# Kernel tuning notes

Measured on AMD Instinct MI355X. Metric: run time of the kernel, lower is better.

The kernel has to match this reference:

```python
import jax, jax.numpy as jnp
import numpy as np

B, C, H, W = 16, 512, 64, 64
SCALE = 8
CQK = C // SCALE  # 64
EPS = 1e-6


def setup_inputs() -> dict:
    key = jax.random.key(0)
    ks = jax.random.split(key, 8)
    x = jax.random.normal(ks[0], (B, C, H, W), dtype=jnp.float32)
    # 1x1 conv weights stored as [out_ch, in_ch] (kernel_size=1)
    Wq = jax.random.normal(ks[1], (CQK, C), dtype=jnp.float32) * 0.02
    bq = jnp.zeros((CQK,), dtype=jnp.float32)
    Wk = jax.random.normal(ks[2], (CQK, C), dtype=jnp.float32) * 0.02
    bk = jnp.zeros((CQK,), dtype=jnp.float32)
    Wv = jax.random.normal(ks[3], (C, C), dtype=jnp.float32) * 0.02
    bv = jnp.zeros((C,), dtype=jnp.float32)
    # gamma is initialized to 0 in the module; use a nonzero value so the
    # output is non-trivial for kernel correctness checks.
    gamma = jax.random.normal(ks[4], (1,), dtype=jnp.float32)
    return {"x": x, "Wq": Wq, "bq": bq, "Wk": Wk, "bk": bk,
            "Wv": Wv, "bv": bv, "gamma": gamma}


def _l2norm_ch(t):
    # normalize over the channel axis (dim=-2), matching torch.norm(p=2, dim=-2)
    nrm = jnp.sqrt(jnp.sum(t * t, axis=-2, keepdims=True))
    return t / jnp.maximum(nrm, EPS)


def reference(x, Wq, bq, Wk, bk, Wv, bv, gamma):
    b, c, h, w = x.shape
    n = h * w
    xf = x.reshape(b, c, n)                                   # [B,C,N]
    # 1x1 convs == channel matmuls
    Q = jnp.einsum('oc,bcn->bon', Wq, xf) + bq[None, :, None]  # [B,cqk,N]
    K = jnp.einsum('oc,bcn->bon', Wk, xf) + bk[None, :, None]  # [B,cqk,N]
    V = jnp.einsum('oc,bcn->bon', Wv, xf) + bv[None, :, None]  # [B,C,N]
    Qn = _l2norm_ch(Q).transpose(0, 2, 1)                      # [B,N,cqk]
    Kn = _l2norm_ch(K)                                         # [B,cqk,N]
    # Taylor-softmax surrogate denominator
    denom = n + jnp.einsum('bnc,bc->bn', Qn, Kn.sum(axis=-1))  # [B,N]
    tailor = 1.0 / jnp.maximum(denom, 1e-6)                    # [B,N]
    # KtV accumulation: [B,cqk,C]
    matrix = jnp.einsum('bmn,bcn->bmc', Kn, V)
    value_sum = jnp.sum(V, axis=-1)[:, :, None]                # [B,C,1] -> broadcast
    matrix_sum = value_sum + jnp.einsum('bnm,bmc->bcn', Qn, matrix)  # [B,C,N]
    weight_value = matrix_sum * tailor[:, None, :]             # [B,C,N]
    out = gamma * weight_value.reshape(b, c, h, w)
    return jnp.nan_to_num(out, nan=0.0, posinf=1.0, neginf=-1.0)
```

## Files before the change

kernel.cpp:

```cpp
#include <hip/hip_runtime.h>


typedef __attribute__((ext_vector_type(8))) short short8_t;
typedef __attribute__((ext_vector_type(4))) float f32x4;

__device__ __forceinline__ unsigned short f2bf(float f) {
  union { float f; unsigned u; } v; v.f = f;
  unsigned r = v.u + 0x7FFFu + ((v.u >> 16) & 1u);
  return (unsigned short)(r >> 16);
}
__device__ __forceinline__ float bf2f(unsigned short h) {
  union { unsigned u; float f; } v; v.u = ((unsigned)h) << 16;
  return v.f;
}

#define MFMA(a, b, c) __builtin_amdgcn_mfma_f32_16x16x32_bf16((a), (b), (c), 0, 0, 0)

__global__ void k_prep(const float* __restrict__ Wq, const float* __restrict__ Wk,
                       unsigned short* __restrict__ Wqk) {
  int idx = blockIdx.x * 256 + threadIdx.x;
  int o = idx >> 9, c = idx & 511;
  float v = (o < 64) ? Wq[o * 512 + c] : Wk[(o - 64) * 512 + c];
  Wqk[idx] = f2bf(v);
}

__launch_bounds__(256, 2)
__global__ void k_qk(const float* __restrict__ x, const unsigned short* __restrict__ Wqk,
                     const float* __restrict__ bq, const float* __restrict__ bk,
                     unsigned short* __restrict__ QnT, unsigned short* __restrict__ KnG,
                     float* __restrict__ Ksum) {
  __shared__ __align__(16) unsigned char smem[39424];
  unsigned short* SA = (unsigned short*)smem;
  unsigned short* SB = (unsigned short*)(smem + 10240);
  unsigned short* EQ = (unsigned short*)smem;
  unsigned short* EK = (unsigned short*)(smem + 18432);
  float* ssq   = (float*)(smem + 35840);
  float* invq  = (float*)(smem + 37888);
  float* invk  = (float*)(smem + 38400);
  float* biasL = (float*)(smem + 38912);

  const int t = threadIdx.x;
  const int lane = t & 63, w = t >> 6;
  const int l15 = lane & 15, quad = lane >> 4;
  const int nt = blockIdx.x, b = blockIdx.y;
  const int n0 = nt * 128;
  const float* xb = x + (size_t)b * 512 * 4096;

  if (t < 128) biasL[t] = (t < 64) ? bq[t] : bk[t - 64];

  f32x4 acc[2][8];
#pragma unroll
  for (int i = 0; i < 2; ++i)
#pragma unroll
    for (int j = 0; j < 8; ++j) acc[i][j] = (f32x4){0.f, 0.f, 0.f, 0.f};

  const int nB = t & 127;
  const int cgB = t >> 7;

  for (int kc = 0; kc < 16; ++kc) {
    const int c0 = kc * 32;
    __syncthreads();
#pragma unroll
    for (int p = 0; p < 2; ++p) {
      int idx = t + p * 256;
      int o = idx >> 2, seg = idx & 3;
      *(short8_t*)(SA + o * 40 + seg * 8) =
          *(const short8_t*)(Wqk + o * 512 + c0 + seg * 8);
    }
#pragma unroll
    for (int g = 0; g < 2; ++g) {
      int cb = c0 + cgB * 8 + g * 16;
      const float* src = xb + (size_t)cb * 4096 + n0 + nB;
      short8_t v;
#pragma unroll
      for (int i = 0; i < 8; ++i) v[i] = (short)f2bf(src[(size_t)i * 4096]);
      *(short8_t*)(SB + nB * 40 + cgB * 8 + g * 16) = v;
    }
    __syncthreads();
    short8_t a0 = *(const short8_t*)(SA + (w * 32 + l15) * 40 + quad * 8);
    short8_t a1 = *(const short8_t*)(SA + (w * 32 + 16 + l15) * 40 + quad * 8);
#pragma unroll
    for (int tc = 0; tc < 8; ++tc) {
      short8_t bfr = *(const short8_t*)(SB + (tc * 16 + l15) * 40 + quad * 8);
      acc[0][tc] = MFMA(a0, bfr, acc[0][tc]);
      acc[1][tc] = MFMA(a1, bfr, acc[1][tc]);
    }
  }
  __syncthreads();

#pragma unroll
  for (int trl = 0; trl < 2; ++trl)
#pragma unroll
    for (int reg = 0; reg < 4; ++reg) {
      int o = w * 32 + trl * 16 + quad * 4 + reg;
      float bias = biasL[o];
#pragma unroll
      for (int tc = 0; tc < 8; ++tc) acc[trl][tc][reg] += bias;
    }

#pragma unroll
  for (int tc = 0; tc < 8; ++tc) {
    float v = 0.f;
#pragma unroll
    for (int trl = 0; trl < 2; ++trl)
#pragma unroll
      for (int reg = 0; reg < 4; ++reg) {
        float q = acc[trl][tc][reg];
        v += q * q;
      }
    v += __shfl_xor(v, 16);
    v += __shfl_xor(v, 32);
    if (quad == 0) ssq[w * 128 + tc * 16 + l15] = v;
  }
  __syncthreads();
  if (t < 128) {
    float qs = ssq[t] + ssq[128 + t];
    float ks = ssq[256 + t] + ssq[384 + t];
    invq[t] = 1.0f / fmaxf(sqrtf(qs), 1e-6f);
    invk[t] = 1.0f / fmaxf(sqrtf(ks), 1e-6f);
  }
  __syncthreads();

  if (w < 2) {
#pragma unroll
    for (int trl = 0; trl < 2; ++trl)
#pragma unroll
      for (int tc = 0; tc < 8; ++tc) {
        int n = tc * 16 + l15;
        float inv = invq[n];
#pragma unroll
        for (int reg = 0; reg < 4; ++reg) {
          int o = w * 32 + trl * 16 + quad * 4 + reg;
          EQ[n * 72 + o] = f2bf(acc[trl][tc][reg] * inv);
        }
      }
  } else {
#pragma unroll
    for (int trl = 0; trl < 2; ++trl)
#pragma unroll
      for (int reg = 0; reg < 4; ++reg) {
        int m = (w - 2) * 32 + trl * 16 + quad * 4 + reg;
        float p = 0.f;
#pragma unroll
        for (int tc = 0; tc < 8; ++tc) {
          int n = tc * 16 + l15;
          float val = acc[trl][tc][reg] * invk[n];
          EK[m * 136 + n] = f2bf(val);
          p += val;
        }
        p += __shfl_xor(p, 1);
        p += __shfl_xor(p, 2);
        p += __shfl_xor(p, 4);
        p += __shfl_xor(p, 8);
        if (l15 == 0) atomicAdd(Ksum + b * 64 + m, p);
      }
  }
  __syncthreads();

  unsigned short* qdst = QnT + ((size_t)b * 4096 + n0) * 64;
#pragma unroll
  for (int p = 0; p < 4; ++p) {
    int idx = t + p * 256;
    int row = idx >> 3, seg = idx & 7;
    *(short8_t*)(qdst + row * 64 + seg * 8) = *(const short8_t*)(EQ + row * 72 + seg * 8);
  }
  unsigned short* kdst = KnG + (size_t)b * 64 * 4096 + n0;
#pragma unroll
  for (int p = 0; p < 4; ++p) {
    int idx = t + p * 256;
    int row = idx >> 4, seg = idx & 15;
    *(short8_t*)(kdst + (size_t)row * 4096 + seg * 8) =
        *(const short8_t*)(EK + row * 136 + seg * 8);
  }
}

__launch_bounds__(256, 2)
__global__ void k_t(const float* __restrict__ x, const unsigned short* __restrict__ KnG,
                    float* __restrict__ T, float* __restrict__ xsum) {
  __shared__ __align__(16) unsigned char smem[15360];
  unsigned short* SA = (unsigned short*)smem;
  unsigned short* SB = (unsigned short*)(smem + 5120);
  const int t = threadIdx.x;
  const int lane = t & 63, w = t >> 6;
  const int l15 = lane & 15, quad = lane >> 4;
  const int ns = blockIdx.x, ct = blockIdx.y, b = blockIdx.z;
  const int c0 = ct * 128;
  const float* xb = x + (size_t)b * 512 * 4096;
  const unsigned short* Knb = KnG + (size_t)b * 64 * 4096;

  f32x4 acc[4][2];
#pragma unroll
  for (int i = 0; i < 4; ++i)
#pragma unroll
    for (int j = 0; j < 2; ++j) acc[i][j] = (f32x4){0.f, 0.f, 0.f, 0.f};

  const int crow = t >> 1, half = t & 1;
  float xs = 0.f;

  for (int ch = 0; ch < 16; ++ch) {
    const int nb = ns * 512 + ch * 32;
    __syncthreads();
    {
      int m = t >> 2, seg = t & 3;
      *(short8_t*)(SA + m * 40 + seg * 8) =
          *(const short8_t*)(Knb + (size_t)m * 4096 + nb + seg * 8);
    }
    {
      const float* src = xb + (size_t)(c0 + crow) * 4096 + nb + half * 16;
      const f32x4* s4 = (const f32x4*)src;
      f32x4 f0 = s4[0], f1 = s4[1], f2 = s4[2], f3 = s4[3];
      short8_t v0, v1;
#pragma unroll
      for (int i = 0; i < 4; ++i) { xs += f0[i]; v0[i] = (short)f2bf(f0[i]); }
#pragma unroll
      for (int i = 0; i < 4; ++i) { xs += f1[i]; v0[4 + i] = (short)f2bf(f1[i]); }
#pragma unroll
      for (int i = 0; i < 4; ++i) { xs += f2[i]; v1[i] = (short)f2bf(f2[i]); }
#pragma unroll
      for (int i = 0; i < 4; ++i) { xs += f3[i]; v1[4 + i] = (short)f2bf(f3[i]); }
      *(short8_t*)(SB + crow * 40 + half * 16)     = v0;
      *(short8_t*)(SB + crow * 40 + half * 16 + 8) = v1;
    }
    __syncthreads();
    short8_t af[4];
#pragma unroll
    for (int tm = 0; tm < 4; ++tm)
      af[tm] = *(const short8_t*)(SA + (tm * 16 + l15) * 40 + quad * 8);
#pragma unroll
    for (int tcl = 0; tcl < 2; ++tcl) {
      short8_t bfr = *(const short8_t*)(SB + (w * 32 + tcl * 16 + l15) * 40 + quad * 8);
#pragma unroll
      for (int tm = 0; tm < 4; ++tm) acc[tm][tcl] = MFMA(af[tm], bfr, acc[tm][tcl]);
    }
  }
  xs += __shfl_xor(xs, 1);
  if (half == 0) atomicAdd(xsum + b * 512 + c0 + crow, xs);
#pragma unroll
  for (int tm = 0; tm < 4; ++tm)
#pragma unroll
    for (int tcl = 0; tcl < 2; ++tcl)
#pragma unroll
      for (int reg = 0; reg < 4; ++reg) {
        int m = tm * 16 + quad * 4 + reg;
        int c = c0 + w * 32 + tcl * 16 + l15;
        atomicAdd(T + ((size_t)b * 64 + m) * 512 + c, acc[tm][tcl][reg]);
      }
}

__launch_bounds__(256, 2)
__global__ void k_mat(const float* __restrict__ T, const float* __restrict__ Wv,
                      const float* __restrict__ bv, const float* __restrict__ xsum,
                      const float* __restrict__ Ksum,
                      unsigned short* __restrict__ matT, float* __restrict__ Vsum) {
  __shared__ __align__(16) unsigned char smem[27136];
  float* ST = (float*)smem;
  float* SW = (float*)(smem + 17408);
  float* SV = (float*)(smem + 26112);
  const int t = threadIdx.x;
  const int cb = blockIdx.x, b = blockIdx.y;
  const int c0 = cb * 32;
  const int m = t >> 2, cs = t & 3;
  float acc[8] = {0.f, 0.f, 0.f, 0.f, 0.f, 0.f, 0.f, 0.f};

  for (int kc = 0; kc < 8; ++kc) {
    __syncthreads();
#pragma unroll
    for (int p = 0; p < 4; ++p) {
      int idx = t + p * 256;
      int row = idx >> 4, f4 = idx & 15;
      *(f32x4*)(ST + row * 68 + f4 * 4) =
          *(const f32x4*)(T + ((size_t)b * 64 + row) * 512 + kc * 64 + f4 * 4);
    }
#pragma unroll
    for (int p = 0; p < 2; ++p) {
      int idx = t + p * 256;
      int row = idx >> 4, f4 = idx & 15;
      *(f32x4*)(SW + row * 68 + f4 * 4) =
          *(const f32x4*)(Wv + (size_t)(c0 + row) * 512 + kc * 64 + f4 * 4);
    }
    __syncthreads();
    for (int kk = 0; kk < 64; ++kk) {
      float tv = ST[m * 68 + kk];
#pragma unroll
      for (int j = 0; j < 8; ++j) acc[j] += tv * SW[(cs + j * 4) * 68 + kk];
    }
  }
  float ks = Ksum[b * 64 + m];
#pragma unroll
  for (int j = 0; j < 8; ++j) {
    int c = c0 + cs + j * 4;
    float mv = acc[j] + bv[c] * ks;
    matT[((size_t)b * 512 + c) * 64 + m] = f2bf(mv);
  }
  {
    int cc = t >> 3, kp = t & 7;
    const float* wr = Wv + (size_t)(c0 + cc) * 512 + kp * 64;
    const float* xr = xsum + b * 512 + kp * 64;
    float s = 0.f;
    for (int i = 0; i < 64; ++i) s += wr[i] * xr[i];
    SV[cc * 8 + kp] = s;
  }
  __syncthreads();
  if (t < 32) {
    float s = 0.f;
#pragma unroll
    for (int i = 0; i < 8; ++i) s += SV[t * 8 + i];
    int c = c0 + t;
    Vsum[b * 512 + c] = s + 4096.0f * bv[c];
  }
}

__launch_bounds__(256, 2)
__global__ void k_out(const unsigned short* __restrict__ QnT,
                      const unsigned short* __restrict__ matT,
                      const float* __restrict__ Ksum, const float* __restrict__ Vsum,
                      const float* __restrict__ gamma, float* __restrict__ out) {
  __shared__ __align__(16) unsigned char smem[38144];
  unsigned short* SA = (unsigned short*)smem;
  unsigned short* SB = (unsigned short*)(smem + 18432);
  float* Ksl  = (float*)(smem + 36864);
  float* tail = (float*)(smem + 37120);
  float* vs   = (float*)(smem + 37632);
  const int t = threadIdx.x;
  const int lane = t & 63, w = t >> 6;
  const int l15 = lane & 15, quad = lane >> 4;
  const int nt = blockIdx.x, ct = blockIdx.y, b = blockIdx.z;
  const int n0 = nt * 128, c0 = ct * 128;

  const unsigned short* asrc = matT + ((size_t)b * 512 + c0) * 64;
  const unsigned short* bsrc = QnT + ((size_t)b * 4096 + n0) * 64;
#pragma unroll
  for (int p = 0; p < 4; ++p) {
    int idx = t + p * 256;
    int row = idx >> 3, seg = idx & 7;
    *(short8_t*)(SA + row * 72 + seg * 8) = *(const short8_t*)(asrc + row * 64 + seg * 8);
    *(short8_t*)(SB + row * 72 + seg * 8) = *(const short8_t*)(bsrc + row * 64 + seg * 8);
  }
  if (t < 64) Ksl[t] = Ksum[b * 64 + t];
  if (t >= 128) vs[t - 128] = Vsum[b * 512 + c0 + (t - 128)];
  __syncthreads();
  if (t < 128) {
    float d = 0.f;
#pragma unroll
    for (int mm = 0; mm < 64; ++mm) d += bf2f(SB[t * 72 + mm]) * Ksl[mm];
    tail[t] = 1.0f / fmaxf(4096.0f + d, 1e-6f);
  }

  f32x4 acc[2][8];
#pragma unroll
  for (int i = 0; i < 2; ++i)
#pragma unroll
    for (int j = 0; j < 8; ++j) acc[i][j] = (f32x4){0.f, 0.f, 0.f, 0.f};

#pragma unroll
  for (int s = 0; s < 2; ++s) {
    short8_t a0 = *(const short8_t*)(SA + (w * 32 + l15) * 72 + s * 32 + quad * 8);
    short8_t a1 = *(const short8_t*)(SA + (w * 32 + 16 + l15) * 72 + s * 32 + quad * 8);
#pragma unroll
    for (int tc = 0; tc < 8; ++tc) {
      short8_t bfr = *(const short8_t*)(SB + (tc * 16 + l15) * 72 + s * 32 + quad * 8);
      acc[0][tc] = MFMA(a0, bfr, acc[0][tc]);
      acc[1][tc] = MFMA(a1, bfr, acc[1][tc]);
    }
  }
  __syncthreads();
  const float g = gamma[0];
  float* ob = out + (size_t)b * 512 * 4096;
#pragma unroll
  for (int trl = 0; trl < 2; ++trl)
#pragma unroll
    for (int tc = 0; tc < 8; ++tc) {
      int n = tc * 16 + l15;
      float tl = tail[n] * g;
#pragma unroll
      for (int reg = 0; reg < 4; ++reg) {
        int cl = w * 32 + trl * 16 + quad * 4 + reg;
        float val = tl * (vs[cl] + acc[trl][tc][reg]);
        ob[(size_t)(c0 + cl) * 4096 + n0 + n] = val;
      }
    }
}

extern "C" void kernel_launch(void* const* d_in, const int* in_sizes, int n_in,
                              void* d_out, int out_size, void* d_ws, size_t ws_size,
                              hipStream_t stream) {
  const float* x     = (const float*)d_in[0];
  const float* Wq    = (const float*)d_in[1];
  const float* bq    = (const float*)d_in[2];
  const float* Wk    = (const float*)d_in[3];
  const float* bk    = (const float*)d_in[4];
  const float* Wv    = (const float*)d_in[5];
  const float* bv    = (const float*)d_in[6];
  const float* gamma = (const float*)d_in[7];
  float* out = (float*)d_out;
  char* ws = (char*)d_ws;

  float* T    = (float*)(ws + 0);
  float* xsum = (float*)(ws + 2097152);
  float* Ksum = (float*)(ws + 2129920);
  float* Vsum = (float*)(ws + 2134016);
  unsigned short* Wqk  = (unsigned short*)(ws + 2166784);
  unsigned short* matT = (unsigned short*)(ws + 2297856);
  unsigned short* QnT  = (unsigned short*)(ws + 3346432);
  unsigned short* Kn   = (unsigned short*)(ws + 11735040);

  hipMemsetAsync(ws, 0, 2134016, stream);
  k_prep<<<256, 256, 0, stream>>>(Wq, Wk, Wqk);
  k_qk<<<dim3(32, 16), 256, 0, stream>>>(x, Wqk, bq, bk, QnT, Kn, Ksum);
  k_t<<<dim3(8, 4, 16), 256, 0, stream>>>(x, Kn, T, xsum);
  k_mat<<<dim3(16, 16), 256, 0, stream>>>(T, Wv, bv, xsum, Ksum, matT, Vsum);
  k_out<<<dim3(32, 4, 16), 256, 0, stream>>>(QnT, matT, Ksum, Vsum, gamma, out);
}
```

Measured before the change: 324.1 us.

## Double-buffer LDS tiles with register prefetch in QK and KtV GEMM kernels

Both the QK projection kernel and the K^T·X accumulation kernel now double-buffer their LDS tiles and prefetch the next K-chunk of global data into registers while the current chunk runs on MFMA. The K-step also doubles from 32 to 64, which halves the iteration count and the number of barriers. The aim is to hide global load latency behind compute. The cost is much more LDS (about 77KB and 55KB per block) and many more registers for the prefetch buffers, which may limit occupancy or cause spills.

```diff
diff --git a/kernel.cpp b/kernel.cpp
--- a/kernel.cpp
+++ b/kernel.cpp
@@ -29,15 +29,17 @@
                      const float* __restrict__ bq, const float* __restrict__ bk,
                      unsigned short* __restrict__ QnT, unsigned short* __restrict__ KnG,
                      float* __restrict__ Ksum) {
-  __shared__ __align__(16) unsigned char smem[39424];
-  unsigned short* SA = (unsigned short*)smem;
-  unsigned short* SB = (unsigned short*)(smem + 10240);
-  unsigned short* EQ = (unsigned short*)smem;
+  __shared__ __align__(16) unsigned char smem[77312];
+  unsigned short* SAb[2] = {(unsigned short*)(smem + 0),
+                            (unsigned short*)(smem + 18432)};
+  unsigned short* SBb[2] = {(unsigned short*)(smem + 36864),
+                            (unsigned short*)(smem + 55296)};
+  unsigned short* EQ = (unsigned short*)(smem + 0);
   unsigned short* EK = (unsigned short*)(smem + 18432);
-  float* ssq   = (float*)(smem + 35840);
-  float* invq  = (float*)(smem + 37888);
-  float* invk  = (float*)(smem + 38400);
-  float* biasL = (float*)(smem + 38912);
+  float* ssq   = (float*)(smem + 73728);
+  float* invq  = (float*)(smem + 75776);
+  float* invk  = (float*)(smem + 76288);
+  float* biasL = (float*)(smem + 76800);
 
   const int t = threadIdx.x;
   const int lane = t & 63, w = t >> 6;
@@ -56,35 +58,61 @@
 
   const int nB = t & 127;
   const int cgB = t >> 7;
-
-  for (int kc = 0; kc < 16; ++kc) {
-    const int c0 = kc * 32;
+  const float* bsrc0 = xb + (size_t)(cgB * 32) * 4096 + n0 + nB;
+
+  short8_t apre[4];
+  float bpre[32];
+
+#define QK_LOADA(kc_) do {                                                     \
+    const int c0_ = (kc_) * 64;                                                \
+    _Pragma("unroll")                                                          \
+    for (int p = 0; p < 4; ++p) {                                              \
+      int gid = t + p * 256; int o_ = gid >> 3, cg = gid & 7;                  \
+      apre[p] = *(const short8_t*)(Wqk + o_ * 512 + c0_ + cg * 8);             \
+    } } while (0)
+
+#define QK_LOADB(kc_) do {                                                     \
+    const float* s_ = bsrc0 + (size_t)(kc_) * 64 * 4096;                       \
+    _Pragma("unroll")                                                          \
+    for (int i = 0; i < 32; ++i) bpre[i] = s_[(size_t)i * 4096];               \
+    } while (0)
+
+#define QK_STORE(pb) do {                                                      \
+    unsigned short* SAp = SAb[pb]; unsigned short* SBp = SBb[pb];              \
+    _Pragma("unroll")                                                          \
+    for (int p = 0; p < 4; ++p) {                                              \
+      int gid = t + p * 256; int o_ = gid >> 3, cg = gid & 7;                  \
+      *(short8_t*)(SAp + o_ * 72 + cg * 8) = apre[p];                          \
+    }                                                                          \
+    _Pragma("unroll")                                                          \
+    for (int j = 0; j < 4; ++j) {                                              \
+      short8_t v_;                                                             \
+      _Pragma("unroll")                                                        \
+      for (int e = 0; e < 8; ++e) v_[e] = (short)f2bf(bpre[j * 8 + e]);        \
+      *(short8_t*)(SBp + nB * 72 + cgB * 32 + j * 8) = v_;                     \
+    } } while (0)
+
+#define QK_MM(pb) do {                                                         \
+    const unsigned short* SAp = SAb[pb]; const unsigned short* SBp = SBb[pb];  \
+    _Pragma("unroll")                                                          \
+    for (int s = 0; s < 2; ++s) {                                              \
+      short8_t a0 = *(const short8_t*)(SAp + (w * 32 + l15) * 72 + s * 32 + quad * 8);      \
+      short8_t a1 = *(const short8_t*)(SAp + (w * 32 + 16 + l15) * 72 + s * 32 + quad * 8); \
+      _Pragma("unroll")                                                        \
+      for (int tc = 0; tc < 8; ++tc) {                                         \
+        short8_t bf_ = *(const short8_t*)(SBp + (tc * 16 + l15) * 72 + s * 32 + quad * 8);  \
+        acc[0][tc] = MFMA(a0, bf_, acc[0][tc]);                                \
+        acc[1][tc] = MFMA(a1, bf_, acc[1][tc]);                                \
+      } } } while (0)
+
+  QK_LOADA(0); QK_LOADB(0);
+#pragma unroll
+  for (int kc = 0; kc < 8; ++kc) {
+    const int pb = kc & 1;
+    QK_STORE(pb);
+    if (kc < 7) { QK_LOADA(kc + 1); QK_LOADB(kc + 1); }
     __syncthreads();
-#pragma unroll
-    for (int p = 0; p < 2; ++p) {
-      int idx = t + p * 256;
-      int o = idx >> 2, seg = idx & 3;
-      *(short8_t*)(SA + o * 40 + seg * 8) =
-          *(const short8_t*)(Wqk + o * 512 + c0 + seg * 8);
-    }
-#pragma unroll
-    for (int g = 0; g < 2; ++g) {
-      int cb = c0 + cgB * 8 + g * 16;
-      const float* src = xb + (size_t)cb * 4096 + n0 + nB;
-      short8_t v;
-#pragma unroll
-      for (int i = 0; i < 8; ++i) v[i] = (short)f2bf(src[(size_t)i * 4096]);
-      *(short8_t*)(SB + nB * 40 + cgB * 8 + g * 16) = v;
-    }
-    __syncthreads();
-    short8_t a0 = *(const short8_t*)(SA + (w * 32 + l15) * 40 + quad * 8);
-    short8_t a1 = *(const short8_t*)(SA + (w * 32 + 16 + l15) * 40 + quad * 8);
-#pragma unroll
-    for (int tc = 0; tc < 8; ++tc) {
-      short8_t bfr = *(const short8_t*)(SB + (tc * 16 + l15) * 40 + quad * 8);
-      acc[0][tc] = MFMA(a0, bfr, acc[0][tc]);
-      acc[1][tc] = MFMA(a1, bfr, acc[1][tc]);
-    }
+    QK_MM(pb);
   }
   __syncthreads();
 
@@ -172,21 +200,27 @@
     *(short8_t*)(kdst + (size_t)row * 4096 + seg * 8) =
         *(const short8_t*)(EK + row * 136 + seg * 8);
   }
+#undef QK_LOADA
+#undef QK_LOADB
+#undef QK_STORE
+#undef QK_MM
 }
 
 __launch_bounds__(256, 2)
 __global__ void k_t(const float* __restrict__ x, const unsigned short* __restrict__ KnG,
                     float* __restrict__ T, float* __restrict__ xsum) {
-  __shared__ __align__(16) unsigned char smem[15360];
-  unsigned short* SA = (unsigned short*)smem;
-  unsigned short* SB = (unsigned short*)(smem + 5120);
+  __shared__ __align__(16) unsigned char smem[55296];
+  unsigned short* SAb[2] = {(unsigned short*)(smem + 0),
+                            (unsigned short*)(smem + 9216)};
+  unsigned short* SBb[2] = {(unsigned short*)(smem + 18432),
+                            (unsigned short*)(smem + 36864)};
   const int t = threadIdx.x;
   const int lane = t & 63, w = t >> 6;
   const int l15 = lane & 15, quad = lane >> 4;
   const int ns = blockIdx.x, ct = blockIdx.y, b = blockIdx.z;
   const int c0 = ct * 128;
   const float* xb = x + (size_t)b * 512 * 4096;
-  const unsigned short* Knb = KnG + (size_t)b * 64 * 4096;
+  const unsigned short* Knb = KnG + (size_t)b * 64 * 4096 + ns * 512;
 
   f32x4 acc[4][2];
 #pragma unroll
@@ -194,47 +228,72 @@
 #pragma unroll
     for (int j = 0; j < 2; ++j) acc[i][j] = (f32x4){0.f, 0.f, 0.f, 0.f};
 
-  const int crow = t >> 1, half = t & 1;
+  const int row = t >> 1, half = t & 1;
   float xs = 0.f;
-
-  for (int ch = 0; ch < 16; ++ch) {
-    const int nb = ns * 512 + ch * 32;
+  const float* bbase = xb + (size_t)(c0 + row) * 4096 + ns * 512 + half * 32;
+
+  short8_t apre[2];
+  f32x4 bpre[8];
+
+#define T_LOADA(ch_) do {                                                      \
+    _Pragma("unroll")                                                          \
+    for (int p = 0; p < 2; ++p) {                                              \
+      int gid = t + p * 256; int m_ = gid >> 3, cg = gid & 7;                  \
+      apre[p] = *(const short8_t*)(Knb + (size_t)m_ * 4096 + (ch_) * 64 + cg * 8); \
+    } } while (0)
+
+#define T_LOADB(ch_) do {                                                      \
+    const float* s_ = bbase + (ch_) * 64;                                      \
+    _Pragma("unroll")                                                          \
+    for (int q = 0; q < 8; ++q) bpre[q] = *(const f32x4*)(s_ + q * 4);         \
+    } while (0)
+
+#define T_STORE(pb) do {                                                       \
+    unsigned short* SAp = SAb[pb]; unsigned short* SBp = SBb[pb];              \
+    _Pragma("unroll")                                                          \
+    for (int p = 0; p < 2; ++p) {                                              \
+      int gid = t + p * 256; int m_ = gid >> 3, cg = gid & 7;                  \
+      *(short8_t*)(SAp + m_ * 72 + cg * 8) = apre[p];                          \
+    }                                                                          \
+    _Pragma("unroll")                                                          \
+    for (int j = 0; j < 4; ++j) {                                              \
+      short8_t v_;                                                             \
+      _Pragma("unroll")                                                        \
+      for (int e = 0; e < 4; ++e) {                                            \
+        float f0 = bpre[j * 2][e], f1 = bpre[j * 2 + 1][e];                    \
+        xs += f0 + f1;                                                         \
+        v_[e] = (short)f2bf(f0); v_[4 + e] = (short)f2bf(f1);                  \
+      }                                                                        \
+      *(short8_t*)(SBp + row * 72 + half * 32 + j * 8) = v_;                   \
+    } } while (0)
+
+#define T_MM(pb) do {                                                          \
+    const unsigned short* SAp = SAb[pb]; const unsigned short* SBp = SBb[pb];  \
+    _Pragma("unroll")                                                          \
+    for (int s = 0; s < 2; ++s) {                                              \
+      short8_t af[4];                                                          \
+      _Pragma("unroll")                                                        \
+      for (int tm = 0; tm < 4; ++tm)                                           \
+        af[tm] = *(const short8_t*)(SAp + (tm * 16 + l15) * 72 + s * 32 + quad * 8); \
+      _Pragma("unroll")                                                        \
+      for (int tcl = 0; tcl < 2; ++tcl) {                                      \
+        short8_t bf_ = *(const short8_t*)(SBp + (w * 32 + tcl * 16 + l15) * 72 + s * 32 + quad * 8); \
+        _Pragma("unroll")                                                      \
+        for (int tm = 0; tm < 4; ++tm) acc[tm][tcl] = MFMA(af[tm], bf_, acc[tm][tcl]); \
+      } } } while (0)
+
+  T_LOADA(0); T_LOADB(0);
+#pragma unroll
+  for (int ch = 0; ch < 8; ++ch) {
+    const int pb = ch & 1;
+    T_STORE(pb);
+    if (ch < 7) { T_LOADA(ch + 1); T_LOADB(ch + 1); }
     __syncthreads();
-    {
-      int m = t >> 2, seg = t & 3;
-      *(short8_t*)(SA + m * 40 + seg * 8) =
-          *(const short8_t*)(Knb + (size_t)m * 4096 + nb + seg * 8);
-    }
-    {
-      const float* src = xb + (size_t)(c0 + crow) * 4096 + nb + half * 16;
-      const f32x4* s4 = (const f32x4*)src;
-      f32x4 f0 = s4[0], f1 = s4[1], f2 = s4[2], f3 = s4[3];
-      short8_t v0, v1;
-#pragma unroll
-      for (int i = 0; i < 4; ++i) { xs += f0[i]; v0[i] = (short)f2bf(f0[i]); }
-#pragma unroll
-      for (int i = 0; i < 4; ++i) { xs += f1[i]; v0[4 + i] = (short)f2bf(f1[i]); }
-#pragma unroll
-      for (int i = 0; i < 4; ++i) { xs += f2[i]; v1[i] = (short)f2bf(f2[i]); }
-#pragma unroll
-      for (int i = 0; i < 4; ++i) { xs += f3[i]; v1[4 + i] = (short)f2bf(f3[i]); }
-      *(short8_t*)(SB + crow * 40 + half * 16)     = v0;
-      *(short8_t*)(SB + crow * 40 + half * 16 + 8) = v1;
-    }
-    __syncthreads();
-    short8_t af[4];
-#pragma unroll
-    for (int tm = 0; tm < 4; ++tm)
-      af[tm] = *(const short8_t*)(SA + (tm * 16 + l15) * 40 + quad * 8);
-#pragma unroll
-    for (int tcl = 0; tcl < 2; ++tcl) {
-      short8_t bfr = *(const short8_t*)(SB + (w * 32 + tcl * 16 + l15) * 40 + quad * 8);
-#pragma unroll
-      for (int tm = 0; tm < 4; ++tm) acc[tm][tcl] = MFMA(af[tm], bfr, acc[tm][tcl]);
-    }
-  }
+    T_MM(pb);
+  }
+
   xs += __shfl_xor(xs, 1);
-  if (half == 0) atomicAdd(xsum + b * 512 + c0 + crow, xs);
+  if (half == 0) atomicAdd(xsum + b * 512 + c0 + row, xs);
 #pragma unroll
   for (int tm = 0; tm < 4; ++tm)
 #pragma unroll
@@ -245,6 +304,10 @@
         int c = c0 + w * 32 + tcl * 16 + l15;
         atomicAdd(T + ((size_t)b * 64 + m) * 512 + c, acc[tm][tcl][reg]);
       }
+#undef T_LOADA
+#undef T_LOADB
+#undef T_STORE
+#undef T_MM
 }
 
 __launch_bounds__(256, 2)
```

Result: no change. 322.9 us (-0.4%).
